# Kernel tuning notes

Hardware: AMD Instinct MI355X
Metric: run time of the kernel (lower is better)

The kernel has to match this reference:

```python
import jax, jax.numpy as jnp
import numpy as np

N_NODES = 50000
N_EDGES = 800000
IN_F = 256
OUT_F = 128
ALPHA = 0.2  # LeakyReLU negative slope


def setup_inputs() -> dict:
    key = jax.random.key(0)
    k_h, k_row, k_col, k_W, k_a = jax.random.split(key, 5)
    h = jax.random.normal(k_h, (N_NODES, IN_F), dtype=jnp.float32)
    row = jax.random.randint(k_row, (N_EDGES,), 0, N_NODES)
    # Guarantee every node appears as a destination so unique(dst) == arange(N)
    col = jnp.concatenate([
        jnp.arange(N_NODES),
        jax.random.randint(k_col, (N_EDGES - N_NODES,), 0, N_NODES),
    ])
    adj = jnp.stack([row, col]).astype(jnp.int64)
    # Xavier-uniform-ish params (gain 1.414)
    lim_W = 1.414 * np.sqrt(6.0 / (IN_F + OUT_F))
    W = jax.random.uniform(k_W, (IN_F, OUT_F), minval=-lim_W, maxval=lim_W, dtype=jnp.float32)
    lim_a = 1.414 * np.sqrt(6.0 / (2 * OUT_F + 1))
    a = jax.random.uniform(k_a, (2 * OUT_F, 1), minval=-lim_a, maxval=lim_a, dtype=jnp.float32)
    return {"h": h, "adj": adj, "W": W, "a": a}


def reference(h, adj, W, a):
    N = h.shape[0]
    self_loops = jnp.arange(N)  # == unique(adj[1]) by input construction
    row = jnp.concatenate([adj[0], self_loops])  # [E_total]
    col = jnp.concatenate([adj[1], self_loops])  # [E_total]

    Wh = h @ W                                    # [N, OUT_F]
    s_src = (Wh @ a[:OUT_F]).squeeze(-1)          # [N] (Wh1)
    s_dst = (Wh @ a[OUT_F:]).squeeze(-1)          # [N] (Wh2)

    e = jax.nn.leaky_relu(s_dst[col] + s_src[row], negative_slope=ALPHA)  # [E_total]

    # segment softmax over destination nodes
    e_max = jax.ops.segment_max(e, col, num_segments=N)
    ex = jnp.exp(e - e_max[col])
    denom = jax.ops.segment_sum(ex, col, num_segments=N)
    att = ex / denom[col]                         # [E_total]

    h_prime = jax.ops.segment_sum(Wh[row] * att[:, None], col, num_segments=N)  # [N, OUT_F]
    return jax.nn.elu(h_prime)  # concat=True
```

## Files before the change

kernel.cpp:

```cpp
#include <hip/hip_runtime.h>
#include <math.h>

#define N_NODES 50000
#define N_EDGES 800000
#define IN_F 256
#define OUT_F 128
#define ALPHA 0.2f
#define SLOT_CAP 64
#define CNT_STRIDE 16

#define NODE_BLOCKS ((N_NODES + 255) / 256)
#define GEMM_WAVES (2 * ((N_NODES + 15) / 16))
#define GEMM_BLOCKS ((GEMM_WAVES + 3) / 4)
#define SCAT_THREADS (N_EDGES / 4)
#define SCAT_BLOCKS ((SCAT_THREADS + 255) / 256)
#define TOT_BLOCKS 2346

typedef short bf16x8 __attribute__((ext_vector_type(8)));
typedef float f32x4  __attribute__((ext_vector_type(4)));

static __device__ __forceinline__ unsigned short f2bf(float f) {
    unsigned int u = __float_as_uint(f);
    u += 0x7FFFu + ((u >> 16) & 1u);
    return (unsigned short)(u >> 16);
}
static __device__ __forceinline__ float bf2f(unsigned int u16) {
    return __uint_as_float(u16 << 16);
}

__global__ __launch_bounds__(256) void k_prep(const float* __restrict__ W,
                                              const float* __restrict__ a,
                                              int* __restrict__ cnt,
                                              float* __restrict__ Wa,
                                              unsigned short* __restrict__ WbT) {
    const int b = blockIdx.x, t = threadIdx.x;
    if (b < NODE_BLOCKS) {
        int i = b * 256 + t;
        if (i < N_NODES) {
            int4 z = make_int4(0, 0, 0, 0);
            int4* p = (int4*)(cnt + (size_t)i * CNT_STRIDE);
            p[0] = z; p[1] = z; p[2] = z; p[3] = z;
        }
    } else if (b == NODE_BLOCKS) {
        const int k = t;
        const float4* wr  = (const float4*)(W + (size_t)k * OUT_F);
        const float4* av1 = (const float4*)a;
        const float4* av2 = (const float4*)(a + OUT_F);
        float s1 = 0.0f, s2 = 0.0f;
#pragma unroll 8
        for (int i = 0; i < OUT_F / 4; ++i) {
            float4 w = wr[i], x = av1[i], y = av2[i];
            s1 = fmaf(w.x, x.x, fmaf(w.y, x.y, fmaf(w.z, x.z, fmaf(w.w, x.w, s1))));
            s2 = fmaf(w.x, y.x, fmaf(w.y, y.y, fmaf(w.z, y.z, fmaf(w.w, y.w, s2))));
        }
        Wa[k] = s1;
        Wa[IN_F + k] = s2;
    } else {
        const int n = b - (NODE_BLOCKS + 1);
        WbT[(size_t)n * IN_F + t] = f2bf(W[(size_t)t * OUT_F + n]);
    }
}

__global__ __launch_bounds__(256) void k_main(const float* __restrict__ h,
                                              const unsigned short* __restrict__ WbT,
                                              const float* __restrict__ Wa,
                                              const int* __restrict__ adj,
                                              unsigned short* __restrict__ Whb,
                                              float* __restrict__ s_src,
                                              float* __restrict__ s_dst,
                                              int* __restrict__ cnt,
                                              unsigned short* __restrict__ slots) {
    const int b = blockIdx.x;
    if (b % 3 == 2) {
        const int sid = b / 3;
        const int t = sid * 256 + threadIdx.x;
        if (t >= SCAT_THREADS) return;
        const int4 s4 = ((const int4*)adj)[t];
        const int4 d4 = ((const int4*)(adj + N_EDGES))[t];
        const int p0 = atomicAdd(&cnt[(size_t)d4.x * CNT_STRIDE], 1);
        const int p1 = atomicAdd(&cnt[(size_t)d4.y * CNT_STRIDE], 1);
        const int p2 = atomicAdd(&cnt[(size_t)d4.z * CNT_STRIDE], 1);
        const int p3 = atomicAdd(&cnt[(size_t)d4.w * CNT_STRIDE], 1);
        if (p0 < SLOT_CAP) slots[(size_t)d4.x * SLOT_CAP + p0] = (unsigned short)s4.x;
        if (p1 < SLOT_CAP) slots[(size_t)d4.y * SLOT_CAP + p1] = (unsigned short)s4.y;
        if (p2 < SLOT_CAP) slots[(size_t)d4.z * SLOT_CAP + p2] = (unsigned short)s4.z;
        if (p3 < SLOT_CAP) slots[(size_t)d4.w * SLOT_CAP + p3] = (unsigned short)s4.w;
        return;
    }
    const int gid = b - b / 3;
    if (gid >= GEMM_BLOCKS) return;
    const int wid = gid * 4 + (threadIdx.x >> 6);
    if (wid >= GEMM_WAVES) return;
    const int lane = threadIdx.x & 63;
    const int m = lane & 15, grp = lane >> 4;
    const int row  = (wid >> 1) * 16 + m;
    const int half = wid & 1;
    const unsigned short* wbase = WbT + (size_t)(half * 64 + m) * IN_F + grp * 8;
    const float* hrow = h + (size_t)row * IN_F + grp * 8;

    f32x4 acc[4];
#pragma unroll
    for (int nt = 0; nt < 4; ++nt) acc[nt] = (f32x4){0.f, 0.f, 0.f, 0.f};
    float sp1 = 0.0f, sp2 = 0.0f;

#pragma unroll
    for (int kt = 0; kt < 8; ++kt) {
        const int k0 = kt * 32;
        const float4* hp = (const float4*)(hrow + k0);
        float4 x0 = hp[0], x1 = hp[1];
        if (half == 0) {
            const float4* wap1 = (const float4*)(Wa + k0 + grp * 8);
            const float4* wap2 = (const float4*)(Wa + IN_F + k0 + grp * 8);
            float4 a0 = wap1[0], a1 = wap1[1];
            float4 b0 = wap2[0], b1 = wap2[1];
            sp1 = fmaf(x0.x, a0.x, fmaf(x0.y, a0.y, fmaf(x0.z, a0.z, fmaf(x0.w, a0.w, sp1))));
            sp1 = fmaf(x1.x, a1.x, fmaf(x1.y, a1.y, fmaf(x1.z, a1.z, fmaf(x1.w, a1.w, sp1))));
            sp2 = fmaf(x0.x, b0.x, fmaf(x0.y, b0.y, fmaf(x0.z, b0.z, fmaf(x0.w, b0.w, sp2))));
            sp2 = fmaf(x1.x, b1.x, fmaf(x1.y, b1.y, fmaf(x1.z, b1.z, fmaf(x1.w, b1.w, sp2))));
        }
        bf16x8 hf;
        hf[0] = (short)f2bf(x0.x); hf[1] = (short)f2bf(x0.y);
        hf[2] = (short)f2bf(x0.z); hf[3] = (short)f2bf(x0.w);
        hf[4] = (short)f2bf(x1.x); hf[5] = (short)f2bf(x1.y);
        hf[6] = (short)f2bf(x1.z); hf[7] = (short)f2bf(x1.w);
#pragma unroll
        for (int nt = 0; nt < 4; ++nt) {
            bf16x8 wf = *(const bf16x8*)(wbase + (size_t)nt * 16 * IN_F + k0);
            acc[nt] = __builtin_amdgcn_mfma_f32_16x16x32_bf16(wf, hf, acc[nt], 0, 0, 0);
        }
    }

    if (half == 0) {
        float t1 = sp1, t2 = sp2;
        t1 += __shfl_xor(t1, 16); t1 += __shfl_xor(t1, 32);
        t2 += __shfl_xor(t2, 16); t2 += __shfl_xor(t2, 32);
        if (grp == 0) { s_src[row] = t1; s_dst[row] = t2; }
    }

    unsigned short* orow = Whb + (size_t)row * OUT_F + half * 64;
#pragma unroll
    for (int nt = 0; nt < 4; ++nt) {
        f32x4 v = acc[nt];
        ushort4 pk;
        pk.x = f2bf(v[0]); pk.y = f2bf(v[1]);
        pk.z = f2bf(v[2]); pk.w = f2bf(v[3]);
        *(ushort4*)(orow + nt * 16 + grp * 4) = pk;
    }
}

__global__ __launch_bounds__(256) void k_gather(const unsigned short* __restrict__ Whb,
                                                const int* __restrict__ cnt,
                                                const unsigned short* __restrict__ slots,
                                                const float* __restrict__ s_src,
                                                const float* __restrict__ s_dst,
                                                float* __restrict__ out) {
    const int wid  = (blockIdx.x * blockDim.x + threadIdx.x) >> 6;
    const int lane = threadIdx.x & 63;
    const int grp  = lane >> 4;
    const int l    = lane & 15;
    const int node = wid * 4 + grp;
    if (node >= N_NODES) return;

    const float sd = s_dst[node];
    float s0 = sd + s_src[node];
    float lr0 = (s0 > 0.0f) ? s0 : ALPHA * s0;
    float x0 = __expf(lr0);
    uint4 w0 = ((const uint4*)(Whb + (size_t)node * OUT_F))[l];
    float a0 = x0 * bf2f(w0.x & 0xFFFFu);
    float a1 = x0 * bf2f(w0.x >> 16);
    float a2 = x0 * bf2f(w0.y & 0xFFFFu);
    float a3 = x0 * bf2f(w0.y >> 16);
    float a4 = x0 * bf2f(w0.z & 0xFFFFu);
    float a5 = x0 * bf2f(w0.z >> 16);
    float a6 = x0 * bf2f(w0.w & 0xFFFFu);
    float a7 = x0 * bf2f(w0.w >> 16);
    float dsum = x0;

    const int deg = min(cnt[(size_t)node * CNT_STRIDE], SLOT_CAP);
    const unsigned short* __restrict__ srow = slots + (size_t)node * SLOT_CAP;

    for (int i = 0; i < deg; i += 8) {
        const uint4 q = *(const uint4*)(srow + i);
        unsigned su[8];
        su[0] = q.x & 0xFFFFu; su[1] = q.x >> 16;
        su[2] = q.y & 0xFFFFu; su[3] = q.y >> 16;
        su[4] = q.z & 0xFFFFu; su[5] = q.z >> 16;
        su[6] = q.w & 0xFFFFu; su[7] = q.w >> 16;
#pragma unroll
        for (int j = 0; j < 8; ++j) su[j] = min(su[j], N_NODES - 1u);
        float e[8];
#pragma unroll
        for (int j = 0; j < 8; ++j) e[j] = sd + s_src[su[j]];
        uint4 v[8];
#pragma unroll
        for (int j = 0; j < 8; ++j) v[j] = ((const uint4*)(Whb + (size_t)su[j] * OUT_F))[l];
        float x[8];
#pragma unroll
        for (int j = 0; j < 8; ++j) {
            float lr = (e[j] > 0.0f) ? e[j] : ALPHA * e[j];
            float xv = __expf(lr);
            x[j] = (i + j < deg) ? xv : 0.0f;
        }
#pragma unroll
        for (int j = 0; j < 8; ++j) dsum += x[j];
#pragma unroll
        for (int j = 0; j < 8; ++j) {
            a0 = fmaf(x[j], bf2f(v[j].x & 0xFFFFu), a0);
            a1 = fmaf(x[j], bf2f(v[j].x >> 16), a1);
            a2 = fmaf(x[j], bf2f(v[j].y & 0xFFFFu), a2);
            a3 = fmaf(x[j], bf2f(v[j].y >> 16), a3);
            a4 = fmaf(x[j], bf2f(v[j].z & 0xFFFFu), a4);
            a5 = fmaf(x[j], bf2f(v[j].z >> 16), a5);
            a6 = fmaf(x[j], bf2f(v[j].w & 0xFFFFu), a6);
            a7 = fmaf(x[j], bf2f(v[j].w >> 16), a7);
        }
    }

    const float inv = 1.0f / dsum;
    float4 o0, o1;
    o0.x = a0 * inv; o0.y = a1 * inv; o0.z = a2 * inv; o0.w = a3 * inv;
    o1.x = a4 * inv; o1.y = a5 * inv; o1.z = a6 * inv; o1.w = a7 * inv;
    o0.x = (o0.x > 0.0f) ? o0.x : expm1f(o0.x);
    o0.y = (o0.y > 0.0f) ? o0.y : expm1f(o0.y);
    o0.z = (o0.z > 0.0f) ? o0.z : expm1f(o0.z);
    o0.w = (o0.w > 0.0f) ? o0.w : expm1f(o0.w);
    o1.x = (o1.x > 0.0f) ? o1.x : expm1f(o1.x);
    o1.y = (o1.y > 0.0f) ? o1.y : expm1f(o1.y);
    o1.z = (o1.z > 0.0f) ? o1.z : expm1f(o1.z);
    o1.w = (o1.w > 0.0f) ? o1.w : expm1f(o1.w);
    float4* op = (float4*)(out + (size_t)node * OUT_F + l * 8);
    op[0] = o0;
    op[1] = o1;
}

extern "C" void kernel_launch(void* const* d_in, const int* in_sizes, int n_in,
                              void* d_out, int out_size, void* d_ws, size_t ws_size,
                              hipStream_t stream) {
    const float* h   = (const float*)d_in[0];
    const int*   adj = (const int*)d_in[1];
    const float* W   = (const float*)d_in[2];
    const float* a   = (const float*)d_in[3];
    float* out = (float*)d_out;

    char* ws = (char*)d_ws;
    const size_t SZ_WHB = (size_t)N_NODES * OUT_F * 2;
    const size_t SZ_N   = 200704;
    const size_t SZ_CNT = (size_t)N_NODES * CNT_STRIDE * 4;
    unsigned short* Whb = (unsigned short*)(ws);
    float* s_src   = (float*)(ws + SZ_WHB);
    float* s_dst   = (float*)(ws + SZ_WHB + SZ_N);
    int*   cnt     = (int*)  (ws + SZ_WHB + 2 * SZ_N);
    float* Wa      = (float*)(ws + SZ_WHB + 2 * SZ_N + SZ_CNT);
    unsigned short* WbT = (unsigned short*)(ws + SZ_WHB + 2 * SZ_N + SZ_CNT + 2048);
    unsigned short* slots = (unsigned short*)(ws + SZ_WHB + 2 * SZ_N + SZ_CNT + 2048 + 65536);

    (void)in_sizes; (void)n_in; (void)out_size; (void)ws_size;

    k_prep  <<<NODE_BLOCKS + 1 + OUT_F, 256, 0, stream>>>(W, a, cnt, Wa, WbT);
    k_main  <<<TOT_BLOCKS, 256, 0, stream>>>(h, WbT, Wa, adj, Whb, s_src, s_dst, cnt, slots);
    k_gather<<<(N_NODES / 4 * 64) / 256, 256, 0, stream>>>(Whb, cnt, slots,
                                                           s_src, s_dst, out);
}
```

Measured before the change: 202.9 us.

## Replace global-atomic edge scatter with LDS-binned per-range counting and compaction

The edge bucketing no longer uses global atomics on padded per-node counters. Each block now owns a range of destination nodes and one chunk of edges, counts with LDS atomics, and writes into per-chunk capped slot lists plus byte counts. A compaction pass, fused into the GEMM launch, then merges these into the per-node slot list that the gather kernel reads. The cost is that every block scans its whole edge chunk, so the dst array is read 32 times, plus an extra raw-slot buffer. Each per-chunk list is capped at 16, so edges past that cap are dropped.

```diff
diff --git a/kernel.cpp b/kernel.cpp
--- a/kernel.cpp
+++ b/kernel.cpp
@@ -6,15 +6,18 @@
 #define IN_F 256
 #define OUT_F 128
 #define ALPHA 0.2f
+
+#define B_DST 32
+#define B_EDGE 8
+#define R_NODES 1563
+#define CHUNK_E (N_EDGES / B_EDGE)
+#define CAP_C 16
+#define SCAT_BLOCKS (B_DST * B_EDGE)
 #define SLOT_CAP 64
-#define CNT_STRIDE 16
-
-#define NODE_BLOCKS ((N_NODES + 255) / 256)
+
+#define COMPACT_BLOCKS ((N_NODES + 255) / 256)
 #define GEMM_WAVES (2 * ((N_NODES + 15) / 16))
 #define GEMM_BLOCKS ((GEMM_WAVES + 3) / 4)
-#define SCAT_THREADS (N_EDGES / 4)
-#define SCAT_BLOCKS ((SCAT_THREADS + 255) / 256)
-#define TOT_BLOCKS 2346
 
 typedef short bf16x8 __attribute__((ext_vector_type(8)));
 typedef float f32x4  __attribute__((ext_vector_type(4)));
@@ -30,18 +33,55 @@
 
 __global__ __launch_bounds__(256) void k_prep(const float* __restrict__ W,
                                               const float* __restrict__ a,
-                                              int* __restrict__ cnt,
+                                              const int* __restrict__ adj,
                                               float* __restrict__ Wa,
-                                              unsigned short* __restrict__ WbT) {
+                                              unsigned short* __restrict__ WbT,
+                                              unsigned short* __restrict__ slots_raw,
+                                              unsigned char* __restrict__ cnt8) {
     const int b = blockIdx.x, t = threadIdx.x;
-    if (b < NODE_BLOCKS) {
-        int i = b * 256 + t;
-        if (i < N_NODES) {
-            int4 z = make_int4(0, 0, 0, 0);
-            int4* p = (int4*)(cnt + (size_t)i * CNT_STRIDE);
-            p[0] = z; p[1] = z; p[2] = z; p[3] = z;
-        }
-    } else if (b == NODE_BLOCKS) {
+    if (b < SCAT_BLOCKS) {
+        const int di = b / B_EDGE;
+        const int j  = b % B_EDGE;
+        const int base = di * R_NODES;
+        const int lim  = min(base + R_NODES, N_NODES);
+        const int nr   = lim - base;
+        __shared__ int cl[R_NODES];
+        for (int k = t; k < R_NODES; k += 256) cl[k] = 0;
+        __syncthreads();
+        const int e0 = j * CHUNK_E;
+        const int4* dp = (const int4*)(adj + N_EDGES + e0);
+        for (int it = t; it < CHUNK_E / 4; it += 256) {
+            const int4 d = dp[it];
+            const int eb = e0 + it * 4;
+            if (d.x >= base && d.x < lim) {
+                const int p = atomicAdd(&cl[d.x - base], 1);
+                if (p < CAP_C)
+                    slots_raw[(size_t)d.x * (B_EDGE * CAP_C) + j * CAP_C + p] =
+                        (unsigned short)adj[eb + 0];
+            }
+            if (d.y >= base && d.y < lim) {
+                const int p = atomicAdd(&cl[d.y - base], 1);
+                if (p < CAP_C)
+                    slots_raw[(size_t)d.y * (B_EDGE * CAP_C) + j * CAP_C + p] =
+                        (unsigned short)adj[eb + 1];
+            }
+            if (d.z >= base && d.z < lim) {
+                const int p = atomicAdd(&cl[d.z - base], 1);
+                if (p < CAP_C)
+                    slots_raw[(size_t)d.z * (B_EDGE * CAP_C) + j * CAP_C + p] =
+                        (unsigned short)adj[eb + 2];
+            }
+            if (d.w >= base && d.w < lim) {
+                const int p = atomicAdd(&cl[d.w - base], 1);
+                if (p < CAP_C)
+                    slots_raw[(size_t)d.w * (B_EDGE * CAP_C) + j * CAP_C + p] =
+                        (unsigned short)adj[eb + 3];
+            }
+        }
+        __syncthreads();
+        for (int k = t; k < nr; k += 256)
+            cnt8[(size_t)(base + k) * B_EDGE + j] = (unsigned char)min(cl[k], CAP_C);
+    } else if (b == SCAT_BLOCKS) {
         const int k = t;
         const float4* wr  = (const float4*)(W + (size_t)k * OUT_F);
         const float4* av1 = (const float4*)a;
@@ -56,39 +96,41 @@
         Wa[k] = s1;
         Wa[IN_F + k] = s2;
     } else {
-        const int n = b - (NODE_BLOCKS + 1);
+        const int n = b - (SCAT_BLOCKS + 1);
         WbT[(size_t)n * IN_F + t] = f2bf(W[(size_t)t * OUT_F + n]);
     }
 }
 
-__global__ __launch_bounds__(256) void k_main(const float* __restrict__ h,
+__global__ __launch_bounds__(256) void k_gemm(const float* __restrict__ h,
                                               const unsigned short* __restrict__ WbT,
                                               const float* __restrict__ Wa,
-                                              const int* __restrict__ adj,
                                               unsigned short* __restrict__ Whb,
                                               float* __restrict__ s_src,
                                               float* __restrict__ s_dst,
-                                              int* __restrict__ cnt,
-                                              unsigned short* __restrict__ slots) {
+                                              const unsigned short* __restrict__ slots_raw,
+                                              const unsigned char* __restrict__ cnt8,
+                                              unsigned short* __restrict__ slots_c,
+                                              int* __restrict__ cntT) {
     const int b = blockIdx.x;
-    if (b % 3 == 2) {
-        const int sid = b / 3;
-        const int t = sid * 256 + threadIdx.x;
-        if (t >= SCAT_THREADS) return;
-        const int4 s4 = ((const int4*)adj)[t];
-        const int4 d4 = ((const int4*)(adj + N_EDGES))[t];
-        const int p0 = atomicAdd(&cnt[(size_t)d4.x * CNT_STRIDE], 1);
-        const int p1 = atomicAdd(&cnt[(size_t)d4.y * CNT_STRIDE], 1);
-        const int p2 = atomicAdd(&cnt[(size_t)d4.z * CNT_STRIDE], 1);
-        const int p3 = atomicAdd(&cnt[(size_t)d4.w * CNT_STRIDE], 1);
-        if (p0 < SLOT_CAP) slots[(size_t)d4.x * SLOT_CAP + p0] = (unsigned short)s4.x;
-        if (p1 < SLOT_CAP) slots[(size_t)d4.y * SLOT_CAP + p1] = (unsigned short)s4.y;
-        if (p2 < SLOT_CAP) slots[(size_t)d4.z * SLOT_CAP + p2] = (unsigned short)s4.z;
-        if (p3 < SLOT_CAP) slots[(size_t)d4.w * SLOT_CAP + p3] = (unsigned short)s4.w;
+    if (b < COMPACT_BLOCKS) {
+        const int node = b * 256 + threadIdx.x;
+        if (node >= N_NODES) return;
+        const unsigned char* c8 = cnt8 + (size_t)node * B_EDGE;
+        const unsigned short* srcrow = slots_raw + (size_t)node * (B_EDGE * CAP_C);
+        unsigned short* drow = slots_c + (size_t)node * SLOT_CAP;
+        int total = 0;
+#pragma unroll
+        for (int c = 0; c < B_EDGE; ++c) {
+            const int dc = c8[c];
+            const unsigned short* s = srcrow + c * CAP_C;
+            for (int k = 0; k < dc; ++k) {
+                if (total < SLOT_CAP) drow[total++] = s[k];
+            }
+        }
+        cntT[node] = total;
         return;
     }
-    const int gid = b - b / 3;
-    if (gid >= GEMM_BLOCKS) return;
+    const int gid = b - COMPACT_BLOCKS;
     const int wid = gid * 4 + (threadIdx.x >> 6);
     if (wid >= GEMM_WAVES) return;
     const int lane = threadIdx.x & 63;
@@ -149,8 +191,8 @@
 }
 
 __global__ __launch_bounds__(256) void k_gather(const unsigned short* __restrict__ Whb,
-                                                const int* __restrict__ cnt,
-                                                const unsigned short* __restrict__ slots,
+                                                const int* __restrict__ cntT,
+                                                const unsigned short* __restrict__ slots_c,
                                                 const float* __restrict__ s_src,
                                                 const float* __restrict__ s_dst,
                                                 float* __restrict__ out) {
@@ -176,8 +218,8 @@
     float a7 = x0 * bf2f(w0.w >> 16);
     float dsum = x0;
 
-    const int deg = min(cnt[(size_t)node * CNT_STRIDE], SLOT_CAP);
-    const unsigned short* __restrict__ srow = slots + (size_t)node * SLOT_CAP;
+    const int deg = min(cntT[node], SLOT_CAP);
+    const unsigned short* __restrict__ srow = slots_c + (size_t)node * SLOT_CAP;
 
     for (int i = 0; i < deg; i += 8) {
         const uint4 q = *(const uint4*)(srow + i);
@@ -187,7 +229,8 @@
         su[4] = q.z & 0xFFFFu; su[5] = q.z >> 16;
         su[6] = q.w & 0xFFFFu; su[7] = q.w >> 16;
 #pragma unroll
-        for (int j = 0; j < 8; ++j) su[j] = min(su[j], N_NODES - 1u);
+        for (int j = 0; j < 8; ++j)
+            su[j] = (i + j < deg) ? min(su[j], N_NODES - 1u) : (unsigned)node;
         float e[8];
 #pragma unroll
         for (int j = 0; j < 8; ++j) e[j] = sd + s_src[su[j]];
@@ -243,21 +286,28 @@
     float* out = (float*)d_out;
 
     char* ws = (char*)d_ws;
-    const size_t SZ_WHB = (size_t)N_NODES * OUT_F * 2;
-    const size_t SZ_N   = 200704;
-    const size_t SZ_CNT = (size_t)N_NODES * CNT_STRIDE * 4;
-    unsigned short* Whb = (unsigned short*)(ws);
-    float* s_src   = (float*)(ws + SZ_WHB);
-    float* s_dst   = (float*)(ws + SZ_WHB + SZ_N);
-    int*   cnt     = (int*)  (ws + SZ_WHB + 2 * SZ_N);
-    float* Wa      = (float*)(ws + SZ_WHB + 2 * SZ_N + SZ_CNT);
-    unsigned short* WbT = (unsigned short*)(ws + SZ_WHB + 2 * SZ_N + SZ_CNT + 2048);
-    unsigned short* slots = (unsigned short*)(ws + SZ_WHB + 2 * SZ_N + SZ_CNT + 2048 + 65536);
+    const size_t SZ_WHB  = (size_t)N_NODES * OUT_F * 2;
+    const size_t SZ_N    = 200704;
+    const size_t SZ_C8   = 401408;
+    const size_t SZ_RAW  = (size_t)N_NODES * B_EDGE * CAP_C * 2;
+    unsigned short* Whb   = (unsigned short*)(ws);
+    float* s_src          = (float*)(ws + SZ_WHB);
+    float* s_dst          = (float*)(ws + SZ_WHB + SZ_N);
+    int*   cntT           = (int*)  (ws + SZ_WHB + 2 * SZ_N);
+    float* Wa             = (float*)(ws + SZ_WHB + 3 * SZ_N);
+    unsigned short* WbT   = (unsigned short*)(ws + SZ_WHB + 3 * SZ_N + 2048);
+    unsigned char* cnt8   = (unsigned char*)(ws + SZ_WHB + 3 * SZ_N + 2048 + 65536);
+    unsigned short* slots_raw = (unsigned short*)(ws + SZ_WHB + 3 * SZ_N + 2048 + 65536 + SZ_C8);
+    unsigned short* slots_c   = (unsigned short*)(ws + SZ_WHB + 3 * SZ_N + 2048 + 65536 + SZ_C8 + SZ_RAW);
 
     (void)in_sizes; (void)n_in; (void)out_size; (void)ws_size;
 
-    k_prep  <<<NODE_BLOCKS + 1 + OUT_F, 256, 0, stream>>>(W, a, cnt, Wa, WbT);
-    k_main  <<<TOT_BLOCKS, 256, 0, stream>>>(h, WbT, Wa, adj, Whb, s_src, s_dst, cnt, slots);
-    k_gather<<<(N_NODES / 4 * 64) / 256, 256, 0, stream>>>(Whb, cnt, slots,
+    k_prep  <<<SCAT_BLOCKS + 1 + OUT_F, 256, 0, stream>>>(W, a, adj, Wa, WbT,
+                                                          slots_raw, cnt8);
+    k_gemm  <<<COMPACT_BLOCKS + GEMM_BLOCKS, 256, 0, stream>>>(h, WbT, Wa, Whb,
+                                                               s_src, s_dst,
+                                                               slots_raw, cnt8,
+                                                               slots_c, cntT);
+    k_gather<<<(N_NODES / 4 * 64) / 256, 256, 0, stream>>>(Whb, cntT, slots_c,
                                                            s_src, s_dst, out);
 }
```

After: 255.5 us. 25.9% more time.
